# Kernel optimization log

Measured on AMD Instinct MI355X. Metric: run time of the kernel, lower is better.

The kernel has to match this reference:

```python
import jax, jax.numpy as jnp
import numpy as np

B, T, D, U = 64, 512, 1024, 1024


def hard_sigmoid(x):
    # keras hard_sigmoid: clip(0.2*x + 0.5, 0, 1)
    return jnp.clip(0.2 * x + 0.5, 0.0, 1.0)


def setup_inputs() -> dict:
    key = jax.random.key(0)
    ks = jax.random.split(key, 6)
    x = jax.random.normal(ks[0], (B, T, D), jnp.float32)
    # glorot-ish scaled params
    kernel = jax.random.normal(ks[1], (D, 4 * U), jnp.float32) * (1.0 / np.sqrt(D).astype(np.float32))
    recurrent_kernel = jax.random.normal(ks[2], (U, 4 * U), jnp.float32) * (1.0 / np.sqrt(U).astype(np.float32))
    peephole_kernel = jax.random.normal(ks[3], (U, 3 * U), jnp.float32) * (1.0 / np.sqrt(U).astype(np.float32))
    projection_kernel = jax.random.normal(ks[4], (U, U), jnp.float32) * (1.0 / np.sqrt(U).astype(np.float32))
    # unit_forget_bias: [zeros(U), ones(U), zeros(2U)] for (i, f, c, o)
    bias = jnp.concatenate([jnp.zeros((U,), jnp.float32), jnp.ones((U,), jnp.float32), jnp.zeros((2 * U,), jnp.float32)])
    h0 = jnp.zeros((B, U), jnp.float32)
    c0 = jnp.zeros((B, U), jnp.float32)
    return {"x": x, "h0": h0, "c0": c0, "kernel": kernel, "recurrent_kernel": recurrent_kernel,
            "peephole_kernel": peephole_kernel, "projection_kernel": projection_kernel, "bias": bias}


def reference(x, h0, c0, kernel, recurrent_kernel, peephole_kernel, projection_kernel, bias):
    U_ = h0.shape[-1]
    Pi = peephole_kernel[:, :U_]
    Pf = peephole_kernel[:, U_:2 * U_]
    Po = peephole_kernel[:, 2 * U_:3 * U_]

    def step(carry, x_t):
        h, c = carry
        # fused gate pre-activations: [B, 4U]
        z = x_t @ kernel + h @ recurrent_kernel + bias
        zi, zf, zc, zo = jnp.split(z, 4, axis=-1)
        i = hard_sigmoid(zi + c @ Pi)            # input gate w/ peephole on c_{t-1}
        f = hard_sigmoid(zf + c @ Pf)            # forget gate w/ peephole on c_{t-1}
        c_new = f * c + i * jnp.tanh(zc)
        o = hard_sigmoid(zo + c_new @ Po)        # output gate w/ peephole on c_t
        # residual LSTM: project tanh(c_t), add residual input, gate by o
        h_new = o * (jnp.tanh(c_new) @ projection_kernel + x_t)
        return (h_new, c_new), h_new

    xs = jnp.swapaxes(x, 0, 1)  # [T, B, D]
    (_, _), hs = jax.lax.scan(step, (h0, c0), xs)
    return jnp.swapaxes(hs, 0, 1)  # [B, T, U]
```

## Files before the change

kernel.cpp:

```cpp
#include <hip/hip_runtime.h>
#include <cstdint>
#include <cstddef>

#define NB 64
#define NT 512
#define ND 1024
#define NU 1024

typedef short s16x8 __attribute__((ext_vector_type(8)));
typedef float f32x4 __attribute__((ext_vector_type(4)));
typedef unsigned int u32x2 __attribute__((ext_vector_type(2)));
typedef unsigned short u16;

__device__ __forceinline__ u16 f2bf(float f) {
  unsigned int u = __float_as_uint(f);
  u += 0x7fffu + ((u >> 16) & 1u);
  return (u16)(u >> 16);
}
__device__ __forceinline__ float bf2f(u16 s) {
  return __uint_as_float(((unsigned int)s) << 16);
}
__device__ __forceinline__ float hsig(float x) {
  return fminf(fmaxf(0.2f * x + 0.5f, 0.0f), 1.0f);
}
__device__ __forceinline__ f32x4 mfma16(s16x8 a, s16x8 b, f32x4 c) {
  return __builtin_amdgcn_mfma_f32_16x16x32_bf16(a, b, c, 0, 0, 0);
}

__device__ __forceinline__ void atomic_swap_u32(unsigned int* p, unsigned int v) {
  asm volatile("global_atomic_swap %0, %1, off" :: "v"(p), "v"(v) : "memory");
}

#define WAIT_VM0() do { \
    asm volatile("s_waitcnt vmcnt(0)" ::: "memory"); \
    __builtin_amdgcn_sched_barrier(0); \
  } while (0)

__global__ __launch_bounds__(256) void xw_gemm(const float* __restrict__ X,
                                               const float* __restrict__ W,
                                               u16* __restrict__ XW) {
  __shared__ u16 Al[128][72];
  __shared__ u16 Bl[128][72];
  const int tid = threadIdx.x;
  const int lane = tid & 63;
  const int wv = tid >> 6;
  const int m0 = (blockIdx.x >> 5) * 128;
  const int n0 = (blockIdx.x & 31) * 128;
  f32x4 acc[4][4];
#pragma unroll
  for (int i = 0; i < 4; ++i)
#pragma unroll
    for (int j = 0; j < 4; ++j) acc[i][j] = (f32x4){0.f, 0.f, 0.f, 0.f};

  for (int kt = 0; kt < 1024; kt += 64) {
    {
      const int r = tid >> 1, hh = (tid & 1) * 32;
      const float* src = X + (size_t)(m0 + r) * 1024 + kt + hh;
      u16* dst = &Al[r][hh];
#pragma unroll
      for (int j = 0; j < 8; ++j) {
        float4 v = ((const float4*)src)[j];
        dst[j * 4 + 0] = f2bf(v.x); dst[j * 4 + 1] = f2bf(v.y);
        dst[j * 4 + 2] = f2bf(v.z); dst[j * 4 + 3] = f2bf(v.w);
      }
    }
    {
      const int kr = tid >> 2, q = (tid & 3) * 32;
      const float* src = W + (size_t)(kt + kr) * 4096 + n0 + q;
#pragma unroll
      for (int j = 0; j < 8; ++j) {
        float4 v = ((const float4*)src)[j];
        const int n = q + j * 4;
        Bl[n + 0][kr] = f2bf(v.x); Bl[n + 1][kr] = f2bf(v.y);
        Bl[n + 2][kr] = f2bf(v.z); Bl[n + 3][kr] = f2bf(v.w);
      }
    }
    __syncthreads();
    const int wm = (wv >> 1) * 64, wn = (wv & 1) * 64;
    const int row = lane & 15, kq = (lane >> 4) * 8;
#pragma unroll
    for (int ks = 0; ks < 2; ++ks) {
      s16x8 af[4], bq[4];
#pragma unroll
      for (int i = 0; i < 4; ++i) af[i] = *(const s16x8*)&Al[wm + i * 16 + row][ks * 32 + kq];
#pragma unroll
      for (int j = 0; j < 4; ++j) bq[j] = *(const s16x8*)&Bl[wn + j * 16 + row][ks * 32 + kq];
#pragma unroll
      for (int i = 0; i < 4; ++i)
#pragma unroll
        for (int j = 0; j < 4; ++j) acc[i][j] = mfma16(af[i], bq[j], acc[i][j]);
    }
    __syncthreads();
  }
  const int wm = (wv >> 1) * 64, wn = (wv & 1) * 64;
  const int col16 = lane & 15, rq = (lane >> 4) * 4;
#pragma unroll
  for (int i = 0; i < 4; ++i)
#pragma unroll
    for (int j = 0; j < 4; ++j)
#pragma unroll
      for (int q = 0; q < 4; ++q) {
        const int m = m0 + wm + i * 16 + rq + q;
        const int n = n0 + wn + j * 16 + col16;
        const int t = m & 511, b = m >> 9;
        const int g = n >> 10, uu = n & 1023;
        const int ugrp = uu >> 3, ul2 = uu & 7;
        XW[(((size_t)ugrp * 512 + t) * 64 + b) * 32 + ul2 * 4 + g] = f2bf(acc[i][j][q]);
      }
}

__global__ void init_comm(const float* __restrict__ h0, const float* __restrict__ c0,
                          u16* hbuf, u16* cbuf) {
  const int i = blockIdx.x * 256 + threadIdx.x;
  hbuf[i] = f2bf(h0[i]);
  cbuf[i] = f2bf(c0[i]);
}

__device__ __forceinline__ void gbar(unsigned int* flags, int bid, int tid, unsigned int ep) {
  __syncthreads();
  if (tid == 0) atomic_swap_u32(flags + bid * 16, ep);
  unsigned int* f = flags + ((((tid & 127) << 1) | (bid & 1)) * 16);
  for (;;) {
    unsigned int v;
    asm volatile("global_load_dword %0, %1, off sc0 sc1\n\ts_waitcnt vmcnt(0)"
                 : "=v"(v) : "v"(f) : "memory");
    if (v >= ep) break;
    __builtin_amdgcn_s_sleep(1);
  }
  __syncthreads();
}

#define WLDS_B   (64 * 1032 * 2)
#define ZOFF     WLDS_B
#define POFF     (ZOFF + 32 * 33 * 4)
#define OOFF     (POFF + 32 * 17 * 4)
#define SMEM_B   (OOFF + 32 * 17 * 4)

__global__ __launch_bounds__(256, 1) void lstm_loop(
    const float* __restrict__ rec, const float* __restrict__ peep,
    const float* __restrict__ projw, const float* __restrict__ bias,
    const float* __restrict__ x, const u16* __restrict__ xw,
    float* __restrict__ out,
    u16* hbuf, u16* cbuf, u16* thbuf,
    unsigned int* flags, const float* __restrict__ c0) {
  extern __shared__ char smem[];
  u16 (*wlds)[1032] = (u16(*)[1032])smem;
  float (*zlds)[33] = (float(*)[33])(smem + ZOFF);
  float (*plds)[17] = (float(*)[17])(smem + POFF);
  float (*olds)[17] = (float(*)[17])(smem + OOFF);

  const int tid = threadIdx.x;
  const int lane = tid & 63;
  const int wv = tid >> 6;
  const int bid = blockIdx.x;
  const int ugrp = bid >> 1;
  const int row0 = (bid & 1) * 32;
  const int u0 = ugrp * 8;

  for (int g = 0; g < 8; ++g) {
    const int c = g * 8 + (tid & 3) * 2;
    const float* sp; int stride, scol;
    if (c < 32)      { sp = rec;   stride = 4096; scol = (c >> 3) * 1024 + u0 + (c & 7); }
    else if (c < 48) { sp = peep;  stride = 3072; scol = ((c - 32) >> 3) * 1024 + u0 + (c & 7); }
    else if (c < 56) { sp = peep;  stride = 3072; scol = 2048 + u0 + (c & 7); }
    else             { sp = projw; stride = 1024; scol = u0 + (c - 56); }
#pragma unroll 4
    for (int p = 0; p < 16; ++p) {
      const int k = p * 64 + (tid >> 2);
      float2 v = *(const float2*)(sp + (size_t)k * stride + scol);
      wlds[c][k] = f2bf(v.x);
      wlds[c + 1][k] = f2bf(v.y);
    }
  }

  const int r = tid >> 3;
  const int ul = tid & 7;
  const int brow = row0 + r;
  const int u = u0 + ul;
  const float b_i = bias[u], b_f = bias[1024 + u], b_c = bias[2048 + u], b_o = bias[3072 + u];
  float cst = c0[brow * 1024 + u];

  const int fcol = lane & 15;
  const int kofs = (lane >> 4) * 8;

  s16x8 av[32];
  u32x2 xwp;
  float xp;

  {
    const u16* xr0 = xw + (((size_t)ugrp * 512 + 0) * 64 + brow) * 32 + ul * 4;
    asm volatile("global_load_dwordx2 %0, %1, off" : "=v"(xwp) : "v"(xr0));
    const float* xs0 = x + (size_t)brow * (512 * 1024) + u;
    asm volatile("global_load_dword %0, %1, off" : "=v"(xp) : "v"(xs0));
  }
  if (wv < 2) {
    const u16* ap = cbuf + (size_t)(row0 + wv * 16 + fcol) * 1024 + kofs;
#pragma unroll
    for (int kt = 0; kt < 32; ++kt)
      asm volatile("global_load_dwordx4 %0, %1, off sc0 sc1"
                   : "=v"(av[kt]) : "v"(ap + kt * 32));
  }
  WAIT_VM0();
  __syncthreads();

  for (int t = 0; t < NT; ++t) {
    float zo_reg, xres, hv;
    const size_t xo = (size_t)brow * (512 * 1024) + (size_t)t * 1024 + u;

    if (wv >= 2) {
      const int rt = wv - 2;
      const u16* ap = hbuf + (size_t)(row0 + rt * 16 + fcol) * 1024 + kofs;
#pragma unroll
      for (int kt = 0; kt < 32; ++kt)
        asm volatile("global_load_dwordx4 %0, %1, off sc0 sc1"
                     : "=v"(av[kt]) : "v"(ap + kt * 32));
      WAIT_VM0();
      f32x4 accA = {0.f, 0.f, 0.f, 0.f}, accB = {0.f, 0.f, 0.f, 0.f};
      const u16* bp0 = &wlds[fcol][kofs];
      const u16* bp1 = &wlds[16 + fcol][kofs];
#pragma unroll
      for (int kt = 0; kt < 32; ++kt) {
        accA = mfma16(av[kt], *(const s16x8*)(bp0 + kt * 32), accA);
        accB = mfma16(av[kt], *(const s16x8*)(bp1 + kt * 32), accB);
      }
      const int srow = rt * 16 + (lane >> 4) * 4;
#pragma unroll
      for (int q = 0; q < 4; ++q) {
        zlds[srow + q][fcol] = accA[q];
        zlds[srow + q][16 + fcol] = accB[q];
      }
    } else {
      f32x4 accP = {0.f, 0.f, 0.f, 0.f};
      const u16* bp = &wlds[32 + fcol][kofs];
#pragma unroll
      for (int kt = 0; kt < 32; ++kt)
        accP = mfma16(av[kt], *(const s16x8*)(bp + kt * 32), accP);
      const int srow = wv * 16 + (lane >> 4) * 4;
#pragma unroll
      for (int q = 0; q < 4; ++q) plds[srow + q][fcol] = accP[q];
    }
    __syncthreads();
    {
      const float xw_i = bf2f((u16)(xwp[0] & 0xffffu));
      const float xw_f = bf2f((u16)(xwp[0] >> 16));
      const float xw_c = bf2f((u16)(xwp[1] & 0xffffu));
      const float xw_o = bf2f((u16)(xwp[1] >> 16));
      xres = xp;
      const float zi = zlds[r][ul]      + xw_i + b_i + plds[r][ul];
      const float zf = zlds[r][8 + ul]  + xw_f + b_f + plds[r][8 + ul];
      const float zc = zlds[r][16 + ul] + xw_c + b_c;
      zo_reg         = zlds[r][24 + ul] + xw_o + b_o;
      const float ig = hsig(zi), fg = hsig(zf);
      cst = fg * cst + ig * tanhf(zc);
      const float th = tanhf(cst);
      const unsigned int cb = f2bf(cst), tb = f2bf(th);
      const unsigned int cpart = (unsigned int)__shfl_xor((int)cb, 1);
      const unsigned int tpart = (unsigned int)__shfl_xor((int)tb, 1);
      if ((ul & 1) == 0) {
        atomic_swap_u32((unsigned int*)(cbuf + brow * 1024 + u), (cpart << 16) | cb);
        atomic_swap_u32((unsigned int*)(thbuf + brow * 1024 + u), (tpart << 16) | tb);
      }
    }
    WAIT_VM0();
    gbar(flags, bid, tid, 2 * t + 1);

    {
      const int prt = wv & 1;
      const u16* ap = ((wv < 2) ? (const u16*)cbuf : (const u16*)thbuf)
                      + (size_t)(row0 + prt * 16 + fcol) * 1024 + kofs;
#pragma unroll
      for (int kt = 0; kt < 32; ++kt)
        asm volatile("global_load_dwordx4 %0, %1, off sc0 sc1"
                     : "=v"(av[kt]) : "v"(ap + kt * 32));
      {
        const int tn = (t + 1 < NT) ? (t + 1) : t;
        const u16* xrn = xw + (((size_t)ugrp * 512 + tn) * 64 + brow) * 32 + ul * 4;
        asm volatile("global_load_dwordx2 %0, %1, off" : "=v"(xwp) : "v"(xrn));
        const float* xsn = x + (size_t)brow * (512 * 1024) + (size_t)tn * 1024 + u;
        asm volatile("global_load_dword %0, %1, off" : "=v"(xp) : "v"(xsn));
      }
      asm volatile("s_waitcnt vmcnt(2)" ::: "memory");
      __builtin_amdgcn_sched_barrier(0);
      f32x4 acc = {0.f, 0.f, 0.f, 0.f};
      const u16* bp = &wlds[48 + fcol][kofs];
#pragma unroll
      for (int kt = 0; kt < 32; ++kt)
        acc = mfma16(av[kt], *(const s16x8*)(bp + kt * 32), acc);
      const int srow = prt * 16 + (lane >> 4) * 4;
      if (wv < 2) {
        if (fcol < 8) {
#pragma unroll
          for (int q = 0; q < 4; ++q) olds[srow + q][fcol] = acc[q];
        }
      } else {
        if (fcol >= 8) {
#pragma unroll
          for (int q = 0; q < 4; ++q) olds[srow + q][fcol] = acc[q];
        }
      }
    }
    __syncthreads();
    {
      const float og = hsig(zo_reg + olds[r][ul]);
      const float pv = olds[r][8 + ul] + xres;
      hv = og * pv;
      const unsigned int hb = f2bf(hv);
      const unsigned int hpart = (unsigned int)__shfl_xor((int)hb, 1);
      if ((ul & 1) == 0)
        atomic_swap_u32((unsigned int*)(hbuf + brow * 1024 + u), (hpart << 16) | hb);
    }
    WAIT_VM0();
    gbar(flags, bid, tid, 2 * t + 2);
    asm volatile("global_store_dword %0, %1, off" :: "v"(out + xo), "v"(hv) : "memory");
  }
}

extern "C" void kernel_launch(void* const* d_in, const int* in_sizes, int n_in,
                              void* d_out, int out_size, void* d_ws, size_t ws_size,
                              hipStream_t stream) {
  const float* x    = (const float*)d_in[0];
  const float* h0   = (const float*)d_in[1];
  const float* c0   = (const float*)d_in[2];
  const float* W    = (const float*)d_in[3];
  const float* R    = (const float*)d_in[4];
  const float* P    = (const float*)d_in[5];
  const float* PRJ  = (const float*)d_in[6];
  const float* bias = (const float*)d_in[7];
  float* out = (float*)d_out;
  char* ws = (char*)d_ws;

  const size_t XW_BYTES = (size_t)32768 * 4096 * 2;
  size_t off = XW_BYTES;
  u16* xw   = (u16*)ws;
  u16* hbuf = (u16*)(ws + off); off += 131072;
  u16* cbuf = (u16*)(ws + off); off += 131072;
  u16* thb  = (u16*)(ws + off); off += 131072;
  unsigned int* flags = (unsigned int*)(ws + off); off += 16384;
  if (ws_size < off) return;

  (void)hipFuncSetAttribute(reinterpret_cast<const void*>(&lstm_loop),
                            hipFuncAttributeMaxDynamicSharedMemorySize, 160 * 1024);

  hipMemsetAsync(flags, 0, 16384, stream);
  hipLaunchKernelGGL(init_comm, dim3(256), dim3(256), 0, stream, h0, c0, hbuf, cbuf);
  hipLaunchKernelGGL(xw_gemm, dim3(8192), dim3(256), 0, stream, x, W, xw);

  void* args[12];
  args[0] = (void*)&R;    args[1] = (void*)&P;     args[2] = (void*)&PRJ;
  args[3] = (void*)&bias; args[4] = (void*)&x;     args[5] = (void*)&xw;
  args[6] = (void*)&out;  args[7] = (void*)&hbuf;  args[8] = (void*)&cbuf;
  args[9] = (void*)&thb;  args[10] = (void*)&flags; args[11] = (void*)&c0;

  hipError_t e = hipLaunchCooperativeKernel((const void*)lstm_loop, dim3(256), dim3(256),
                                            args, (unsigned int)SMEM_B, stream);
  if (e != hipSuccess) {
    hipLaunchKernelGGL(lstm_loop, dim3(256), dim3(256), SMEM_B, stream,
                       R, P, PRJ, bias, x, xw, out, hbuf, cbuf, thb, flags, c0);
  }
}
```

Before: 7.836 ms.

## Stage per-timestep h/c/tanh(c) buffers so cross-block reads avoid cache bypass

Adds a staged variant of the persistent LSTM kernel that writes h, c and tanh(c) to a fresh buffer per timestep instead of reusing one shared buffer. Each address is written only once, so the cross-block reads can use plain loads instead of system-coherent sc0 sc1 loads that bypass cache. The goal is lower latency on the per-step exchange between blocks. It needs about 200MB of extra workspace and falls back to the old path if that space is missing. It also relies on plain loads never returning stale lines for these fresh addresses.

New measurement: 7.389 ms. 1.06x faster.

```diff
diff --git a/kernel.cpp b/kernel.cpp
--- a/kernel.cpp
+++ b/kernel.cpp
@@ -29,6 +29,14 @@
 
 __device__ __forceinline__ void atomic_swap_u32(unsigned int* p, unsigned int v) {
   asm volatile("global_atomic_swap %0, %1, off" :: "v"(p), "v"(v) : "memory");
+}
+
+template <int STAGED>
+__device__ __forceinline__ void ldx4(s16x8& d, const u16* a) {
+  if constexpr (STAGED)
+    asm volatile("global_load_dwordx4 %0, %1, off" : "=v"(d) : "v"(a));
+  else
+    asm volatile("global_load_dwordx4 %0, %1, off sc0 sc1" : "=v"(d) : "v"(a));
 }
 
 #define WAIT_VM0() do { \
@@ -110,10 +118,10 @@
 }
 
 __global__ void init_comm(const float* __restrict__ h0, const float* __restrict__ c0,
-                          u16* hbuf, u16* cbuf) {
+                          u16* hini, u16* cini) {
   const int i = blockIdx.x * 256 + threadIdx.x;
-  hbuf[i] = f2bf(h0[i]);
-  cbuf[i] = f2bf(c0[i]);
+  hini[i] = f2bf(h0[i]);
+  cini[i] = f2bf(c0[i]);
 }
 
 __device__ __forceinline__ void gbar(unsigned int* flags, int bid, int tid, unsigned int ep) {
@@ -135,13 +143,16 @@
 #define POFF     (ZOFF + 32 * 33 * 4)
 #define OOFF     (POFF + 32 * 17 * 4)
 #define SMEM_B   (OOFF + 32 * 17 * 4)
-
+#define STEP_E   65536
+
+template <int STAGED>
 __global__ __launch_bounds__(256, 1) void lstm_loop(
     const float* __restrict__ rec, const float* __restrict__ peep,
     const float* __restrict__ projw, const float* __restrict__ bias,
     const float* __restrict__ x, const u16* __restrict__ xw,
     float* __restrict__ out,
-    u16* hbuf, u16* cbuf, u16* thbuf,
+    u16* hini, u16* cini, u16* thsg,
+    u16* hst, u16* cst, u16* thst,
     unsigned int* flags, const float* __restrict__ c0) {
   extern __shared__ char smem[];
   u16 (*wlds)[1032] = (u16(*)[1032])smem;
@@ -178,7 +189,8 @@
   const int brow = row0 + r;
   const int u = u0 + ul;
   const float b_i = bias[u], b_f = bias[1024 + u], b_c = bias[2048 + u], b_o = bias[3072 + u];
-  float cst = c0[brow * 1024 + u];
+  float cst0 = c0[brow * 1024 + u];
+  float cstv = cst0;
 
   const int fcol = lane & 15;
   const int kofs = (lane >> 4) * 8;
@@ -194,7 +206,7 @@
     asm volatile("global_load_dword %0, %1, off" : "=v"(xp) : "v"(xs0));
   }
   if (wv < 2) {
-    const u16* ap = cbuf + (size_t)(row0 + wv * 16 + fcol) * 1024 + kofs;
+    const u16* ap = cini + (size_t)(row0 + wv * 16 + fcol) * 1024 + kofs;
 #pragma unroll
     for (int kt = 0; kt < 32; ++kt)
       asm volatile("global_load_dwordx4 %0, %1, off sc0 sc1"
@@ -207,13 +219,21 @@
     float zo_reg, xres, hv;
     const size_t xo = (size_t)brow * (512 * 1024) + (size_t)t * 1024 + u;
 
+    const u16* hsrc; u16* cpub; u16* thpub; const u16* csrc; const u16* thsrc; u16* hpub;
+    if constexpr (STAGED) {
+      hsrc  = t ? (hst + (size_t)(t - 1) * STEP_E) : hini;
+      hpub  = hst + (size_t)t * STEP_E;
+      cpub  = cst + (size_t)t * STEP_E;   csrc  = cpub;
+      thpub = thst + (size_t)t * STEP_E;  thsrc = thpub;
+    } else {
+      hsrc = hini; hpub = hini; cpub = cini; csrc = cini; thpub = thsg; thsrc = thsg;
+    }
+
     if (wv >= 2) {
       const int rt = wv - 2;
-      const u16* ap = hbuf + (size_t)(row0 + rt * 16 + fcol) * 1024 + kofs;
-#pragma unroll
-      for (int kt = 0; kt < 32; ++kt)
-        asm volatile("global_load_dwordx4 %0, %1, off sc0 sc1"
-                     : "=v"(av[kt]) : "v"(ap + kt * 32));
+      const u16* ap = hsrc + (size_t)(row0 + rt * 16 + fcol) * 1024 + kofs;
+#pragma unroll
+      for (int kt = 0; kt < 32; ++kt) ldx4<STAGED>(av[kt], ap + kt * 32);
       WAIT_VM0();
       f32x4 accA = {0.f, 0.f, 0.f, 0.f}, accB = {0.f, 0.f, 0.f, 0.f};
       const u16* bp0 = &wlds[fcol][kofs];
@@ -251,14 +271,14 @@
       const float zc = zlds[r][16 + ul] + xw_c + b_c;
       zo_reg         = zlds[r][24 + ul] + xw_o + b_o;
       const float ig = hsig(zi), fg = hsig(zf);
-      cst = fg * cst + ig * tanhf(zc);
-      const float th = tanhf(cst);
-      const unsigned int cb = f2bf(cst), tb = f2bf(th);
+      cstv = fg * cstv + ig * tanhf(zc);
+      const float th = tanhf(cstv);
+      const unsigned int cb = f2bf(cstv), tb = f2bf(th);
       const unsigned int cpart = (unsigned int)__shfl_xor((int)cb, 1);
       const unsigned int tpart = (unsigned int)__shfl_xor((int)tb, 1);
       if ((ul & 1) == 0) {
-        atomic_swap_u32((unsigned int*)(cbuf + brow * 1024 + u), (cpart << 16) | cb);
-        atomic_swap_u32((unsigned int*)(thbuf + brow * 1024 + u), (tpart << 16) | tb);
+        atomic_swap_u32((unsigned int*)(cpub + brow * 1024 + u), (cpart << 16) | cb);
+        atomic_swap_u32((unsigned int*)(thpub + brow * 1024 + u), (tpart << 16) | tb);
       }
     }
     WAIT_VM0();
@@ -266,12 +286,10 @@
 
     {
       const int prt = wv & 1;
-      const u16* ap = ((wv < 2) ? (const u16*)cbuf : (const u16*)thbuf)
+      const u16* ap = ((wv < 2) ? csrc : thsrc)
                       + (size_t)(row0 + prt * 16 + fcol) * 1024 + kofs;
 #pragma unroll
-      for (int kt = 0; kt < 32; ++kt)
-        asm volatile("global_load_dwordx4 %0, %1, off sc0 sc1"
-                     : "=v"(av[kt]) : "v"(ap + kt * 32));
+      for (int kt = 0; kt < 32; ++kt) ldx4<STAGED>(av[kt], ap + kt * 32);
       {
         const int tn = (t + 1 < NT) ? (t + 1) : t;
         const u16* xrn = xw + (((size_t)ugrp * 512 + tn) * 64 + brow) * 32 + ul * 4;
@@ -307,7 +325,7 @@
       const unsigned int hb = f2bf(hv);
       const unsigned int hpart = (unsigned int)__shfl_xor((int)hb, 1);
       if ((ul & 1) == 0)
-        atomic_swap_u32((unsigned int*)(hbuf + brow * 1024 + u), (hpart << 16) | hb);
+        atomic_swap_u32((unsigned int*)(hpub + brow * 1024 + u), (hpart << 16) | hb);
     }
     WAIT_VM0();
     gbar(flags, bid, tid, 2 * t + 2);
@@ -332,29 +350,45 @@
   const size_t XW_BYTES = (size_t)32768 * 4096 * 2;
   size_t off = XW_BYTES;
   u16* xw   = (u16*)ws;
-  u16* hbuf = (u16*)(ws + off); off += 131072;
-  u16* cbuf = (u16*)(ws + off); off += 131072;
-  u16* thb  = (u16*)(ws + off); off += 131072;
+  u16* hini = (u16*)(ws + off); off += 131072;
+  u16* cini = (u16*)(ws + off); off += 131072;
+  u16* thsg = (u16*)(ws + off); off += 131072;
   unsigned int* flags = (unsigned int*)(ws + off); off += 16384;
-  if (ws_size < off) return;
-
-  (void)hipFuncSetAttribute(reinterpret_cast<const void*>(&lstm_loop),
+  const size_t base_need = off;
+  u16* hst = (u16*)(ws + off); off += (size_t)NT * 131072;
+  u16* cst = (u16*)(ws + off); off += (size_t)NT * 131072;
+  u16* thst = (u16*)(ws + off); off += (size_t)NT * 131072;
+  const size_t staged_need = off;
+  if (ws_size < base_need) return;
+  const int staged = (ws_size >= staged_need) ? 1 : 0;
+
+  (void)hipFuncSetAttribute(reinterpret_cast<const void*>(&lstm_loop<1>),
                             hipFuncAttributeMaxDynamicSharedMemorySize, 160 * 1024);
+  (void)hipFuncSetAttribute(reinterpret_cast<const void*>(&lstm_loop<0>),
+                            hipFuncAttributeMaxDynamicSharedMemorySize, 160 * 1024);
 
   hipMemsetAsync(flags, 0, 16384, stream);
-  hipLaunchKernelGGL(init_comm, dim3(256), dim3(256), 0, stream, h0, c0, hbuf, cbuf);
+  hipLaunchKernelGGL(init_comm, dim3(256), dim3(256), 0, stream, h0, c0, hini, cini);
   hipLaunchKernelGGL(xw_gemm, dim3(8192), dim3(256), 0, stream, x, W, xw);
 
-  void* args[12];
-  args[0] = (void*)&R;    args[1] = (void*)&P;     args[2] = (void*)&PRJ;
-  args[3] = (void*)&bias; args[4] = (void*)&x;     args[5] = (void*)&xw;
-  args[6] = (void*)&out;  args[7] = (void*)&hbuf;  args[8] = (void*)&cbuf;
-  args[9] = (void*)&thb;  args[10] = (void*)&flags; args[11] = (void*)&c0;
-
-  hipError_t e = hipLaunchCooperativeKernel((const void*)lstm_loop, dim3(256), dim3(256),
+  void* args[15];
+  args[0] = (void*)&R;     args[1] = (void*)&P;     args[2] = (void*)&PRJ;
+  args[3] = (void*)&bias;  args[4] = (void*)&x;     args[5] = (void*)&xw;
+  args[6] = (void*)&out;   args[7] = (void*)&hini;  args[8] = (void*)&cini;
+  args[9] = (void*)&thsg;  args[10] = (void*)&hst;  args[11] = (void*)&cst;
+  args[12] = (void*)&thst; args[13] = (void*)&flags; args[14] = (void*)&c0;
+
+  const void* fn = staged ? (const void*)&lstm_loop<1> : (const void*)&lstm_loop<0>;
+  hipError_t e = hipLaunchCooperativeKernel(fn, dim3(256), dim3(256),
                                             args, (unsigned int)SMEM_B, stream);
   if (e != hipSuccess) {
-    hipLaunchKernelGGL(lstm_loop, dim3(256), dim3(256), SMEM_B, stream,
-                       R, P, PRJ, bias, x, xw, out, hbuf, cbuf, thb, flags, c0);
-  }
-}
+    if (staged)
+      hipLaunchKernelGGL((lstm_loop<1>), dim3(256), dim3(256), SMEM_B, stream,
+                         R, P, PRJ, bias, x, xw, out, hini, cini, thsg,
+                         hst, cst, thst, flags, c0);
+    else
+      hipLaunchKernelGGL((lstm_loop<0>), dim3(256), dim3(256), SMEM_B, stream,
+                         R, P, PRJ, bias, x, xw, out, hini, cini, thsg,
+                         hst, cst, thst, flags, c0);
+  }
+}
```
